# Kernel tuning notes

Hardware: AMD Instinct MI355X
Metric: run time of the kernel (lower is better)

The kernel has to match this reference:

```python
import jax, jax.numpy as jnp
import numpy as np

N, E = 50000, 400000
FN, FE = 128, 128          # in/out node and edge feature dims
W = 256                     # fnns_width
EPS = 1e-5


def _layer_norm(x, g, b):
    m = x.mean(-1, keepdims=True)
    var = x.var(-1, keepdims=True)
    return (x - m) / jnp.sqrt(var + EPS) * g + b


def _fnn(x, params):
    # FNN applies ReLU after EVERY linear, including the last one.
    for w, b in params:
        x = jax.nn.relu(x @ w + b)
    return x


def setup_inputs() -> dict:
    key = jax.random.key(0)
    ks = jax.random.split(key, 32)
    s = 0.05
    d = {
        'v': jax.random.normal(ks[0], (N, FN), jnp.float32),
        'e': jax.random.normal(ks[1], (E, FE), jnp.float32),
        'edge_index': jax.random.randint(ks[2], (2, E), 0, N, jnp.int32),
        # edge branch: LayerNorm over concat width FE + 2*FN = 384
        'edge_ln_g': jnp.ones((FE + 2 * FN,), jnp.float32),
        'edge_ln_b': jnp.zeros((FE + 2 * FN,), jnp.float32),
        'ew0': jax.random.normal(ks[3], (FE + 2 * FN, W), jnp.float32) * s,
        'eb0': jnp.zeros((W,), jnp.float32),
        'ew1': jax.random.normal(ks[4], (W, W), jnp.float32) * s,
        'eb1': jnp.zeros((W,), jnp.float32),
        'ew2': jax.random.normal(ks[5], (W, FE), jnp.float32) * s,
        'eb2': jnp.zeros((FE,), jnp.float32),
        'edge_linear': jax.random.normal(ks[6], (FE, FE), jnp.float32) * s,
        # node branch: LayerNorm over concat width FE + FN = 256
        'node_ln_g': jnp.ones((FE + FN,), jnp.float32),
        'node_ln_b': jnp.zeros((FE + FN,), jnp.float32),
        'nw0': jax.random.normal(ks[7], (FE + FN, W), jnp.float32) * s,
        'nb0': jnp.zeros((W,), jnp.float32),
        'nw1': jax.random.normal(ks[8], (W, W), jnp.float32) * s,
        'nb1': jnp.zeros((W,), jnp.float32),
        'nw2': jax.random.normal(ks[9], (W, FN), jnp.float32) * s,
        'nb2': jnp.zeros((FN,), jnp.float32),
        'node_linear': jax.random.normal(ks[10], (FN, FN), jnp.float32) * s,
    }
    return d


def reference(v, e, edge_index, edge_ln_g, edge_ln_b, ew0, eb0, ew1, eb1,
              ew2, eb2, edge_linear, node_ln_g, node_ln_b, nw0, nb0, nw1,
              nb1, nw2, nb2, node_linear):
    row, col = edge_index[0], edge_index[1]
    n = v.shape[0]
    # edge update: residual linear + FNN(LayerNorm(concat))
    edge_in = jnp.concatenate([e, v[row], v[col]], axis=-1)  # [E, 384]
    e_new = e @ edge_linear + _fnn(
        _layer_norm(edge_in, edge_ln_g, edge_ln_b),
        [(ew0, eb0), (ew1, eb1), (ew2, eb2)])
    # mean scatter-aggregate over destination nodes (col)
    counts = jax.ops.segment_sum(jnp.ones((e.shape[0],), e.dtype), col,
                                 num_segments=n)
    e_aggr = jax.ops.segment_sum(e_new, col, num_segments=n)
    e_aggr = e_aggr / jnp.clip(counts, 1.0)[:, None]
    # node update
    node_in = jnp.concatenate([e_aggr, v], axis=-1)  # [N, 256]
    v_new = v @ node_linear + _fnn(
        _layer_norm(node_in, node_ln_g, node_ln_b),
        [(nw0, nb0), (nw1, nb1), (nw2, nb2)])
    return (v_new, e_new)
```

## Files before the change

kernel.cpp:

```cpp
#include <hip/hip_runtime.h>

typedef _Float16 f16_t;
typedef f16_t f16x4 __attribute__((ext_vector_type(4)));
typedef f16_t f16x8 __attribute__((ext_vector_type(8)));
typedef float f32x4 __attribute__((ext_vector_type(4)));

#define MFMA16(a, b, c) __builtin_amdgcn_mfma_f32_16x16x32_f16((a), (b), (c), 0, 0, 0)

__device__ __forceinline__ float bfr(float x) { return (float)(__bf16)x; }

__global__ void pack_weights_kernel(
    const float* __restrict__ ew0, const float* __restrict__ ew1,
    const float* __restrict__ ew2, const float* __restrict__ eL,
    const float* __restrict__ nw0, const float* __restrict__ nw1,
    const float* __restrict__ nw2, const float* __restrict__ nL,
    f16_t* __restrict__ dst)
{
    int tid = blockIdx.x * 256 + threadIdx.x;
    int fid = tid >> 6, lane = tid & 63;
    const float* src; int Ncols, foff, doff;
    if (fid < 192)      { src = ew0; Ncols = 256; foff = 0;   doff = 0;      }
    else if (fid < 320) { src = ew1; Ncols = 256; foff = 192; doff = 98304;  }
    else if (fid < 384) { src = ew2; Ncols = 128; foff = 320; doff = 163840; }
    else if (fid < 416) { src = eL;  Ncols = 128; foff = 384; doff = 196608; }
    else if (fid < 544) { src = nw0; Ncols = 256; foff = 416; doff = 212992; }
    else if (fid < 672) { src = nw1; Ncols = 256; foff = 544; doff = 278528; }
    else if (fid < 736) { src = nw2; Ncols = 128; foff = 672; doff = 344064; }
    else                { src = nL;  Ncols = 128; foff = 736; doff = 376832; }
    int f = fid - foff;
    int NT = Ncols >> 4;
    int kstep = f / NT, ntile = f - kstep * NT;
    int col = ntile * 16 + (lane & 15);
    int kbase = kstep * 32 + ((lane >> 4) << 3);
    f16x8 out;
    #pragma unroll
    for (int j = 0; j < 8; ++j)
        out[j] = (f16_t)bfr(src[(size_t)(kbase + j) * Ncols + col]);
    *reinterpret_cast<f16x8*>(dst + (size_t)doff + ((size_t)f * 64 + lane) * 8) = out;
}

__launch_bounds__(1024, 8)
__global__ void edge_kernel(
    const float* __restrict__ vfeat, const float* __restrict__ efeat,
    const int* __restrict__ eidx,
    const float* __restrict__ lng, const float* __restrict__ lnb,
    const f16_t* __restrict__ pw,
    const float* __restrict__ b0, const float* __restrict__ b1,
    const float* __restrict__ b2,
    float* __restrict__ out_e, float* __restrict__ aggr, float* __restrict__ cnts,
    int Ee)
{
    __shared__ f16_t X[64 * 392];
    __shared__ f16_t ER[64 * 136];
    __shared__ int cidx[64];

    const int t    = threadIdx.x;
    const int lane = t & 63;
    const int wv   = t >> 6;
    const size_t ebase = (size_t)blockIdx.x * 64;

    const int el = t >> 4;
    const int pp = t & 15;
    const size_t eg = ebase + el;
    const int r0 = eidx[eg];
    const int c0 = eidx[(size_t)Ee + eg];

    float s = 0.f, sq = 0.f;
    {
        const float4* e4 = (const float4*)efeat;
        const float4* v4 = (const float4*)vfeat;
        #pragma unroll
        for (int i = 0; i < 6; ++i) {
            int q = i * 16 + pp;
            float4 r;
            if (q < 32)      r = e4[eg * 32 + q];
            else if (q < 64) r = v4[(size_t)r0 * 32 + (q - 32)];
            else             r = v4[(size_t)c0 * 32 + (q - 64)];
            r.x = bfr(r.x); r.y = bfr(r.y); r.z = bfr(r.z); r.w = bfr(r.w);
            f16x4 h;
            h[0] = (f16_t)r.x; h[1] = (f16_t)r.y; h[2] = (f16_t)r.z; h[3] = (f16_t)r.w;
            *reinterpret_cast<f16x4*>(&X[el * 392 + q * 4]) = h;
            if (q < 32)
                *reinterpret_cast<f16x4*>(&ER[el * 136 + q * 4]) = h;
            s  += r.x + r.y + r.z + r.w;
            sq += r.x*r.x + r.y*r.y + r.z*r.z + r.w*r.w;
        }
        if (pp == 0) {
            cidx[el] = c0;
            unsafeAtomicAdd(&cnts[c0], 1.0f);
        }
    }
    #pragma unroll
    for (int off = 1; off < 16; off <<= 1) {
        s  += __shfl_xor(s, off);
        sq += __shfl_xor(sq, off);
    }
    const float mean = s * (1.f / 384.f);
    const float rstd = 1.f / sqrtf(sq * (1.f / 384.f) - mean * mean + 1e-5f);

    {
        const float4* g4p = (const float4*)lng;
        const float4* bpp = (const float4*)lnb;
        #pragma unroll
        for (int i = 0; i < 6; ++i) {
            int q = i * 16 + pp;
            f16x4 h = *reinterpret_cast<f16x4*>(&X[el * 392 + q * 4]);
            float4 g = g4p[q]; float4 bb = bpp[q];
            h[0] = (f16_t)(((float)h[0] - mean) * rstd * bfr(g.x) + bfr(bb.x));
            h[1] = (f16_t)(((float)h[1] - mean) * rstd * bfr(g.y) + bfr(bb.y));
            h[2] = (f16_t)(((float)h[2] - mean) * rstd * bfr(g.z) + bfr(bb.z));
            h[3] = (f16_t)(((float)h[3] - mean) * rstd * bfr(g.w) + bfr(bb.w));
            *reinterpret_cast<f16x4*>(&X[el * 392 + q * 4]) = h;
        }
    }
    __syncthreads();

    const int r16 = lane & 15;
    const int g4i = lane >> 4;

    {
        f32x4 acc[4] = {};
        const f16_t* bw = pw;
        #pragma unroll
        for (int ks = 0; ks < 12; ++ks) {
            f16x8 b = *reinterpret_cast<const f16x8*>(
                &bw[((size_t)(ks * 16 + wv) * 64 + lane) * 8]);
            #pragma unroll
            for (int m = 0; m < 4; ++m) {
                f16x8 a = *reinterpret_cast<const f16x8*>(
                    &X[(m * 16 + r16) * 392 + ks * 32 + g4i * 8]);
                acc[m] = MFMA16(a, b, acc[m]);
            }
        }
        __syncthreads();
        int c = wv * 16 + r16;
        float bias = bfr(b0[c]);
        #pragma unroll
        for (int m = 0; m < 4; ++m)
            #pragma unroll
            for (int qi = 0; qi < 4; ++qi) {
                int rr = m * 16 + g4i * 4 + qi;
                X[rr * 264 + c] = (f16_t)fmaxf(acc[m][qi] + bias, 0.f);
            }
    }
    __syncthreads();

    {
        f32x4 acc[4] = {};
        const f16_t* bw = pw + 98304;
        #pragma unroll
        for (int ks = 0; ks < 8; ++ks) {
            f16x8 b = *reinterpret_cast<const f16x8*>(
                &bw[((size_t)(ks * 16 + wv) * 64 + lane) * 8]);
            #pragma unroll
            for (int m = 0; m < 4; ++m) {
                f16x8 a = *reinterpret_cast<const f16x8*>(
                    &X[(m * 16 + r16) * 264 + ks * 32 + g4i * 8]);
                acc[m] = MFMA16(a, b, acc[m]);
            }
        }
        __syncthreads();
        int c = wv * 16 + r16;
        float bias = bfr(b1[c]);
        #pragma unroll
        for (int m = 0; m < 4; ++m)
            #pragma unroll
            for (int qi = 0; qi < 4; ++qi) {
                int rr = m * 16 + g4i * 4 + qi;
                X[rr * 264 + c] = (f16_t)fmaxf(acc[m][qi] + bias, 0.f);
            }
    }
    __syncthreads();

    {
        const int nh = wv & 7;
        const int mh = wv >> 3;
        f32x4 accF[2] = {}, accR[2] = {};
        const f16_t* bw = pw + 163840;
        #pragma unroll
        for (int ks = 0; ks < 8; ++ks) {
            f16x8 b = *reinterpret_cast<const f16x8*>(
                &bw[((size_t)(ks * 8 + nh) * 64 + lane) * 8]);
            #pragma unroll
            for (int m = 0; m < 2; ++m) {
                f16x8 a = *reinterpret_cast<const f16x8*>(
                    &X[(mh * 32 + m * 16 + r16) * 264 + ks * 32 + g4i * 8]);
                accF[m] = MFMA16(a, b, accF[m]);
            }
        }
        const f16_t* bwL = pw + 196608;
        #pragma unroll
        for (int ks = 0; ks < 4; ++ks) {
            f16x8 b = *reinterpret_cast<const f16x8*>(
                &bwL[((size_t)(ks * 8 + nh) * 64 + lane) * 8]);
            #pragma unroll
            for (int m = 0; m < 2; ++m) {
                f16x8 a = *reinterpret_cast<const f16x8*>(
                    &ER[(mh * 32 + m * 16 + r16) * 136 + ks * 32 + g4i * 8]);
                accR[m] = MFMA16(a, b, accR[m]);
            }
        }
        int c = nh * 16 + r16;
        float bias = bfr(b2[c]);
        #pragma unroll
        for (int m = 0; m < 2; ++m)
            #pragma unroll
            for (int qi = 0; qi < 4; ++qi) {
                int rr = mh * 32 + m * 16 + g4i * 4 + qi;
                float val = accR[m][qi] + fmaxf(accF[m][qi] + bias, 0.f);
                size_t eg2 = ebase + rr;
                out_e[eg2 * 128 + c] = val;
                unsafeAtomicAdd(&aggr[(size_t)cidx[rr] * 128 + c], val);
            }
    }
}

__launch_bounds__(512, 6)
__global__ void node_kernel(
    const float* __restrict__ vfeat, const float* __restrict__ aggr,
    const float* __restrict__ cnts,
    const float* __restrict__ lng, const float* __restrict__ lnb,
    const f16_t* __restrict__ pw,
    const float* __restrict__ b0, const float* __restrict__ b1,
    const float* __restrict__ b2,
    float* __restrict__ out_v, int Nn)
{
    __shared__ f16_t X[32 * 264];
    __shared__ f16_t H1[32 * 264];

    const int t    = threadIdx.x;
    const int lane = t & 63;
    const int wv   = t >> 6;
    const size_t nbase = (size_t)blockIdx.x * 32;

    const int nl = t >> 4;
    const int pp = t & 15;
    const size_t ng = nbase + nl;
    const bool valid = ng < (size_t)Nn;

    float4 d[4];
    float s = 0.f, sq = 0.f;
    {
        float cmax = 1.f;
        if (valid) cmax = fmaxf(cnts[ng], 1.f);
        const float4* a4 = (const float4*)aggr;
        const float4* v4 = (const float4*)vfeat;
        #pragma unroll
        for (int i = 0; i < 4; ++i) {
            int q = i * 16 + pp;
            float4 r = make_float4(0.f, 0.f, 0.f, 0.f);
            if (valid) {
                if (q < 32) {
                    r = a4[ng * 32 + q];
                    r.x = r.x / cmax; r.y = r.y / cmax;
                    r.z = r.z / cmax; r.w = r.w / cmax;
                } else {
                    float4 rv = v4[ng * 32 + (q - 32)];
                    r.x = bfr(rv.x); r.y = bfr(rv.y); r.z = bfr(rv.z); r.w = bfr(rv.w);
                }
            }
            d[i] = r;
            s  += r.x + r.y + r.z + r.w;
            sq += r.x*r.x + r.y*r.y + r.z*r.z + r.w*r.w;
        }
    }
    #pragma unroll
    for (int off = 1; off < 16; off <<= 1) {
        s  += __shfl_xor(s, off);
        sq += __shfl_xor(sq, off);
    }
    const float mean = s * (1.f / 256.f);
    const float rstd = 1.f / sqrtf(sq * (1.f / 256.f) - mean * mean + 1e-5f);
    {
        const float4* g4p = (const float4*)lng;
        const float4* bpp = (const float4*)lnb;
        #pragma unroll
        for (int i = 0; i < 4; ++i) {
            int q = i * 16 + pp;
            float4 g = g4p[q]; float4 bb = bpp[q];
            f16x4 y;
            y[0] = (f16_t)((d[i].x - mean) * rstd * bfr(g.x) + bfr(bb.x));
            y[1] = (f16_t)((d[i].y - mean) * rstd * bfr(g.y) + bfr(bb.y));
            y[2] = (f16_t)((d[i].z - mean) * rstd * bfr(g.z) + bfr(bb.z));
            y[3] = (f16_t)((d[i].w - mean) * rstd * bfr(g.w) + bfr(bb.w));
            *reinterpret_cast<f16x4*>(&X[nl * 264 + q * 4]) = y;
        }
    }
    __syncthreads();

    const int r16 = lane & 15;
    const int g4i = lane >> 4;

    {
        f32x4 acc[2][2] = {};
        const f16_t* bw = pw;
        #pragma unroll
        for (int ks = 0; ks < 8; ++ks) {
            f16x8 a0 = *reinterpret_cast<const f16x8*>(&X[r16 * 264 + ks * 32 + g4i * 8]);
            f16x8 a1 = *reinterpret_cast<const f16x8*>(&X[(16 + r16) * 264 + ks * 32 + g4i * 8]);
            #pragma unroll
            for (int n = 0; n < 2; ++n) {
                f16x8 b = *reinterpret_cast<const f16x8*>(
                    &bw[((size_t)(ks * 16 + wv * 2 + n) * 64 + lane) * 8]);
                acc[0][n] = MFMA16(a0, b, acc[0][n]);
                acc[1][n] = MFMA16(a1, b, acc[1][n]);
            }
        }
        #pragma unroll
        for (int n = 0; n < 2; ++n) {
            int c = wv * 32 + n * 16 + r16;
            float bias = bfr(b0[c]);
            #pragma unroll
            for (int m = 0; m < 2; ++m)
                #pragma unroll
                for (int qi = 0; qi < 4; ++qi) {
                    int rr = m * 16 + g4i * 4 + qi;
                    H1[rr * 264 + c] = (f16_t)fmaxf(acc[m][n][qi] + bias, 0.f);
                }
        }
    }
    __syncthreads();

    f16_t* h2 = X;
    {
        f32x4 acc[2][2] = {};
        const f16_t* bw = pw + 65536;
        #pragma unroll
        for (int ks = 0; ks < 8; ++ks) {
            f16x8 a0 = *reinterpret_cast<const f16x8*>(&H1[r16 * 264 + ks * 32 + g4i * 8]);
            f16x8 a1 = *reinterpret_cast<const f16x8*>(&H1[(16 + r16) * 264 + ks * 32 + g4i * 8]);
            #pragma unroll
            for (int n = 0; n < 2; ++n) {
                f16x8 b = *reinterpret_cast<const f16x8*>(
                    &bw[((size_t)(ks * 16 + wv * 2 + n) * 64 + lane) * 8]);
                acc[0][n] = MFMA16(a0, b, acc[0][n]);
                acc[1][n] = MFMA16(a1, b, acc[1][n]);
            }
        }
        __syncthreads();
        #pragma unroll
        for (int n = 0; n < 2; ++n) {
            int c = wv * 32 + n * 16 + r16;
            float bias = bfr(b1[c]);
            #pragma unroll
            for (int m = 0; m < 2; ++m)
                #pragma unroll
                for (int qi = 0; qi < 4; ++qi) {
                    int rr = m * 16 + g4i * 4 + qi;
                    h2[rr * 264 + c] = (f16_t)fmaxf(acc[m][n][qi] + bias, 0.f);
                }
        }
    }
    __syncthreads();

    {
        f32x4 accF[2] = {}, accR[2] = {};
        const f16_t* bw = pw + 131072;
        #pragma unroll
        for (int ks = 0; ks < 8; ++ks) {
            f16x8 a0 = *reinterpret_cast<const f16x8*>(&h2[r16 * 264 + ks * 32 + g4i * 8]);
            f16x8 a1 = *reinterpret_cast<const f16x8*>(&h2[(16 + r16) * 264 + ks * 32 + g4i * 8]);
            f16x8 b = *reinterpret_cast<const f16x8*>(
                &bw[((size_t)(ks * 8 + wv) * 64 + lane) * 8]);
            accF[0] = MFMA16(a0, b, accF[0]);
            accF[1] = MFMA16(a1, b, accF[1]);
        }
        const f16_t* bwL = pw + 163840;
        #pragma unroll
        for (int ks = 0; ks < 4; ++ks) {
            f16x8 a[2];
            #pragma unroll
            for (int m = 0; m < 2; ++m) {
                size_t rv = nbase + (size_t)(m * 16 + r16);
                if (rv >= (size_t)Nn) rv = (size_t)Nn - 1;
                const float* src = &vfeat[rv * 128 + ks * 32 + g4i * 8];
                float4 f0 = *(const float4*)src;
                float4 f1 = *(const float4*)(src + 4);
                f16x8 av;
                av[0] = (f16_t)bfr(f0.x); av[1] = (f16_t)bfr(f0.y);
                av[2] = (f16_t)bfr(f0.z); av[3] = (f16_t)bfr(f0.w);
                av[4] = (f16_t)bfr(f1.x); av[5] = (f16_t)bfr(f1.y);
                av[6] = (f16_t)bfr(f1.z); av[7] = (f16_t)bfr(f1.w);
                a[m] = av;
            }
            f16x8 b = *reinterpret_cast<const f16x8*>(
                &bwL[((size_t)(ks * 8 + wv) * 64 + lane) * 8]);
            accR[0] = MFMA16(a[0], b, accR[0]);
            accR[1] = MFMA16(a[1], b, accR[1]);
        }
        int c = wv * 16 + r16;
        float bias = bfr(b2[c]);
        #pragma unroll
        for (int m = 0; m < 2; ++m)
            #pragma unroll
            for (int qi = 0; qi < 4; ++qi) {
                int rr = m * 16 + g4i * 4 + qi;
                size_t ng2 = nbase + rr;
                if (ng2 < (size_t)Nn) {
                    float val = accR[m][qi] + fmaxf(accF[m][qi] + bias, 0.f);
                    out_v[ng2 * 128 + c] = val;
                }
            }
    }
}

extern "C" void kernel_launch(void* const* d_in, const int* in_sizes, int n_in,
                              void* d_out, int out_size, void* d_ws, size_t ws_size,
                              hipStream_t stream)
{
    const float* v    = (const float*)d_in[0];
    const float* e    = (const float*)d_in[1];
    const int*   eidx = (const int*)d_in[2];
    const float* elng = (const float*)d_in[3];
    const float* elnb = (const float*)d_in[4];
    const float* ew0  = (const float*)d_in[5];
    const float* eb0  = (const float*)d_in[6];
    const float* ew1  = (const float*)d_in[7];
    const float* eb1  = (const float*)d_in[8];
    const float* ew2  = (const float*)d_in[9];
    const float* eb2  = (const float*)d_in[10];
    const float* eLin = (const float*)d_in[11];
    const float* nlng = (const float*)d_in[12];
    const float* nlnb = (const float*)d_in[13];
    const float* nw0  = (const float*)d_in[14];
    const float* nb0  = (const float*)d_in[15];
    const float* nw1  = (const float*)d_in[16];
    const float* nb1  = (const float*)d_in[17];
    const float* nw2  = (const float*)d_in[18];
    const float* nb2  = (const float*)d_in[19];
    const float* nLin = (const float*)d_in[20];

    const int Nn = in_sizes[0] / 128;
    const int Ee = in_sizes[1] / 128;

    float* out_v = (float*)d_out;
    float* out_e = out_v + (size_t)Nn * 128;

    float* aggr = (float*)d_ws;
    float* cnts = aggr + (size_t)Nn * 128;
    f16_t* packw = (f16_t*)((char*)d_ws + (size_t)Nn * 129 * 4);

    hipMemsetAsync(d_ws, 0, (size_t)Nn * 129 * 4, stream);

    pack_weights_kernel<<<192, 256, 0, stream>>>(ew0, ew1, ew2, eLin,
                                                 nw0, nw1, nw2, nLin, packw);

    edge_kernel<<<(Ee + 63) / 64, 1024, 0, stream>>>(v, e, eidx, elng, elnb, packw,
                                                     eb0, eb1, eb2, out_e, aggr, cnts, Ee);

    node_kernel<<<(Nn + 31) / 32, 512, 0, stream>>>(v, aggr, cnts, nlng, nlnb,
                                                    packw + 212992, nb0, nb1, nb2,
                                                    out_v, Nn);
}
```

Baseline: 436.0 us.

## Swap MFMA operands to emit transposed tiles with vectorized stores and drop ER buffer

The MFMA operands are swapped so weights go in the A slot and activations in the B slot. Each lane then holds four consecutive output columns for one row, which allows f16x4 stores into shared memory and float4 stores to global output in place of scalar stores. The edge kernel also drops the ER shared-memory copy of the raw edge features and re-reads them from global memory for the residual linear, which shrinks LDS use and may raise occupancy. The cost is extra global loads for the residual path, and the aggregation atomics now hit four adjacent addresses per lane.

```diff
diff --git a/kernel.cpp b/kernel.cpp
--- a/kernel.cpp
+++ b/kernel.cpp
@@ -51,7 +51,6 @@
     int Ee)
 {
     __shared__ f16_t X[64 * 392];
-    __shared__ f16_t ER[64 * 136];
     __shared__ int cidx[64];
 
     const int t    = threadIdx.x;
@@ -61,9 +60,9 @@
 
     const int el = t >> 4;
     const int pp = t & 15;
-    const size_t eg = ebase + el;
-    const int r0 = eidx[eg];
-    const int c0 = eidx[(size_t)Ee + eg];
+    const size_t eg0 = ebase + el;
+    const int r0 = eidx[eg0];
+    const int c0 = eidx[(size_t)Ee + eg0];
 
     float s = 0.f, sq = 0.f;
     {
@@ -73,15 +72,13 @@
         for (int i = 0; i < 6; ++i) {
             int q = i * 16 + pp;
             float4 r;
-            if (q < 32)      r = e4[eg * 32 + q];
+            if (q < 32)      r = e4[eg0 * 32 + q];
             else if (q < 64) r = v4[(size_t)r0 * 32 + (q - 32)];
             else             r = v4[(size_t)c0 * 32 + (q - 64)];
             r.x = bfr(r.x); r.y = bfr(r.y); r.z = bfr(r.z); r.w = bfr(r.w);
             f16x4 h;
             h[0] = (f16_t)r.x; h[1] = (f16_t)r.y; h[2] = (f16_t)r.z; h[3] = (f16_t)r.w;
             *reinterpret_cast<f16x4*>(&X[el * 392 + q * 4]) = h;
-            if (q < 32)
-                *reinterpret_cast<f16x4*>(&ER[el * 136 + q * 4]) = h;
             s  += r.x + r.y + r.z + r.w;
             sq += r.x*r.x + r.y*r.y + r.z*r.z + r.w*r.w;
         }
@@ -117,31 +114,34 @@
 
     const int r16 = lane & 15;
     const int g4i = lane >> 4;
+    const int cb4 = g4i * 4;
 
     {
         f32x4 acc[4] = {};
         const f16_t* bw = pw;
         #pragma unroll
         for (int ks = 0; ks < 12; ++ks) {
-            f16x8 b = *reinterpret_cast<const f16x8*>(
+            f16x8 wa = *reinterpret_cast<const f16x8*>(
                 &bw[((size_t)(ks * 16 + wv) * 64 + lane) * 8]);
             #pragma unroll
-            for (int m = 0; m < 4; ++m) {
-                f16x8 a = *reinterpret_cast<const f16x8*>(
-                    &X[(m * 16 + r16) * 392 + ks * 32 + g4i * 8]);
-                acc[m] = MFMA16(a, b, acc[m]);
+            for (int et = 0; et < 4; ++et) {
+                f16x8 xb = *reinterpret_cast<const f16x8*>(
+                    &X[(et * 16 + r16) * 392 + ks * 32 + g4i * 8]);
+                acc[et] = MFMA16(wa, xb, acc[et]);
             }
         }
         __syncthreads();
-        int c = wv * 16 + r16;
-        float bias = bfr(b0[c]);
-        #pragma unroll
-        for (int m = 0; m < 4; ++m)
-            #pragma unroll
-            for (int qi = 0; qi < 4; ++qi) {
-                int rr = m * 16 + g4i * 4 + qi;
-                X[rr * 264 + c] = (f16_t)fmaxf(acc[m][qi] + bias, 0.f);
-            }
+        int cb = wv * 16 + cb4;
+        float4 bs = *reinterpret_cast<const float4*>(&b0[cb]);
+        float bias[4] = { bfr(bs.x), bfr(bs.y), bfr(bs.z), bfr(bs.w) };
+        #pragma unroll
+        for (int et = 0; et < 4; ++et) {
+            f16x4 hv;
+            #pragma unroll
+            for (int qi = 0; qi < 4; ++qi)
+                hv[qi] = (f16_t)fmaxf(acc[et][qi] + bias[qi], 0.f);
+            *reinterpret_cast<f16x4*>(&X[(et * 16 + r16) * 264 + cb]) = hv;
+        }
     }
     __syncthreads();
 
@@ -150,25 +150,27 @@
         const f16_t* bw = pw + 98304;
         #pragma unroll
         for (int ks = 0; ks < 8; ++ks) {
-            f16x8 b = *reinterpret_cast<const f16x8*>(
+            f16x8 wa = *reinterpret_cast<const f16x8*>(
                 &bw[((size_t)(ks * 16 + wv) * 64 + lane) * 8]);
             #pragma unroll
-            for (int m = 0; m < 4; ++m) {
-                f16x8 a = *reinterpret_cast<const f16x8*>(
-                    &X[(m * 16 + r16) * 264 + ks * 32 + g4i * 8]);
-                acc[m] = MFMA16(a, b, acc[m]);
+            for (int et = 0; et < 4; ++et) {
+                f16x8 xb = *reinterpret_cast<const f16x8*>(
+                    &X[(et * 16 + r16) * 264 + ks * 32 + g4i * 8]);
+                acc[et] = MFMA16(wa, xb, acc[et]);
             }
         }
         __syncthreads();
-        int c = wv * 16 + r16;
-        float bias = bfr(b1[c]);
-        #pragma unroll
-        for (int m = 0; m < 4; ++m)
-            #pragma unroll
-            for (int qi = 0; qi < 4; ++qi) {
-                int rr = m * 16 + g4i * 4 + qi;
-                X[rr * 264 + c] = (f16_t)fmaxf(acc[m][qi] + bias, 0.f);
-            }
+        int cb = wv * 16 + cb4;
+        float4 bs = *reinterpret_cast<const float4*>(&b1[cb]);
+        float bias[4] = { bfr(bs.x), bfr(bs.y), bfr(bs.z), bfr(bs.w) };
+        #pragma unroll
+        for (int et = 0; et < 4; ++et) {
+            f16x4 hv;
+            #pragma unroll
+            for (int qi = 0; qi < 4; ++qi)
+                hv[qi] = (f16_t)fmaxf(acc[et][qi] + bias[qi], 0.f);
+            *reinterpret_cast<f16x4*>(&X[(et * 16 + r16) * 264 + cb]) = hv;
+        }
     }
     __syncthreads();
 
@@ -179,39 +181,53 @@
         const f16_t* bw = pw + 163840;
         #pragma unroll
         for (int ks = 0; ks < 8; ++ks) {
-            f16x8 b = *reinterpret_cast<const f16x8*>(
+            f16x8 wa = *reinterpret_cast<const f16x8*>(
                 &bw[((size_t)(ks * 8 + nh) * 64 + lane) * 8]);
             #pragma unroll
-            for (int m = 0; m < 2; ++m) {
-                f16x8 a = *reinterpret_cast<const f16x8*>(
-                    &X[(mh * 32 + m * 16 + r16) * 264 + ks * 32 + g4i * 8]);
-                accF[m] = MFMA16(a, b, accF[m]);
+            for (int p = 0; p < 2; ++p) {
+                f16x8 xb = *reinterpret_cast<const f16x8*>(
+                    &X[((mh * 2 + p) * 16 + r16) * 264 + ks * 32 + g4i * 8]);
+                accF[p] = MFMA16(wa, xb, accF[p]);
             }
         }
         const f16_t* bwL = pw + 196608;
         #pragma unroll
         for (int ks = 0; ks < 4; ++ks) {
-            f16x8 b = *reinterpret_cast<const f16x8*>(
+            f16x8 wa = *reinterpret_cast<const f16x8*>(
                 &bwL[((size_t)(ks * 8 + nh) * 64 + lane) * 8]);
             #pragma unroll
-            for (int m = 0; m < 2; ++m) {
-                f16x8 a = *reinterpret_cast<const f16x8*>(
-                    &ER[(mh * 32 + m * 16 + r16) * 136 + ks * 32 + g4i * 8]);
-                accR[m] = MFMA16(a, b, accR[m]);
-            }
-        }
-        int c = nh * 16 + r16;
-        float bias = bfr(b2[c]);
-        #pragma unroll
-        for (int m = 0; m < 2; ++m)
-            #pragma unroll
-            for (int qi = 0; qi < 4; ++qi) {
-                int rr = mh * 32 + m * 16 + g4i * 4 + qi;
-                float val = accR[m][qi] + fmaxf(accF[m][qi] + bias, 0.f);
-                size_t eg2 = ebase + rr;
-                out_e[eg2 * 128 + c] = val;
-                unsafeAtomicAdd(&aggr[(size_t)cidx[rr] * 128 + c], val);
-            }
+            for (int p = 0; p < 2; ++p) {
+                size_t er = ebase + (size_t)((mh * 2 + p) * 16 + r16);
+                const float4* src = (const float4*)&efeat[er * 128 + ks * 32 + g4i * 8];
+                float4 f0 = src[0];
+                float4 f1 = src[1];
+                f16x8 ebf;
+                ebf[0] = (f16_t)bfr(f0.x); ebf[1] = (f16_t)bfr(f0.y);
+                ebf[2] = (f16_t)bfr(f0.z); ebf[3] = (f16_t)bfr(f0.w);
+                ebf[4] = (f16_t)bfr(f1.x); ebf[5] = (f16_t)bfr(f1.y);
+                ebf[6] = (f16_t)bfr(f1.z); ebf[7] = (f16_t)bfr(f1.w);
+                accR[p] = MFMA16(wa, ebf, accR[p]);
+            }
+        }
+        int cb = nh * 16 + cb4;
+        float4 bs = *reinterpret_cast<const float4*>(&b2[cb]);
+        float bias[4] = { bfr(bs.x), bfr(bs.y), bfr(bs.z), bfr(bs.w) };
+        #pragma unroll
+        for (int p = 0; p < 2; ++p) {
+            int rr = (mh * 2 + p) * 16 + r16;
+            size_t eg2 = ebase + rr;
+            float4 val;
+            val.x = accR[p][0] + fmaxf(accF[p][0] + bias[0], 0.f);
+            val.y = accR[p][1] + fmaxf(accF[p][1] + bias[1], 0.f);
+            val.z = accR[p][2] + fmaxf(accF[p][2] + bias[2], 0.f);
+            val.w = accR[p][3] + fmaxf(accF[p][3] + bias[3], 0.f);
+            *reinterpret_cast<float4*>(&out_e[eg2 * 128 + cb]) = val;
+            float* ap = &aggr[(size_t)cidx[rr] * 128 + cb];
+            unsafeAtomicAdd(ap + 0, val.x);
+            unsafeAtomicAdd(ap + 1, val.y);
+            unsafeAtomicAdd(ap + 2, val.z);
+            unsafeAtomicAdd(ap + 3, val.w);
+        }
     }
 }
 
@@ -290,65 +306,73 @@
 
     const int r16 = lane & 15;
     const int g4i = lane >> 4;
+    const int cb4 = g4i * 4;
 
     {
         f32x4 acc[2][2] = {};
         const f16_t* bw = pw;
         #pragma unroll
         for (int ks = 0; ks < 8; ++ks) {
-            f16x8 a0 = *reinterpret_cast<const f16x8*>(&X[r16 * 264 + ks * 32 + g4i * 8]);
-            f16x8 a1 = *reinterpret_cast<const f16x8*>(&X[(16 + r16) * 264 + ks * 32 + g4i * 8]);
-            #pragma unroll
-            for (int n = 0; n < 2; ++n) {
-                f16x8 b = *reinterpret_cast<const f16x8*>(
-                    &bw[((size_t)(ks * 16 + wv * 2 + n) * 64 + lane) * 8]);
-                acc[0][n] = MFMA16(a0, b, acc[0][n]);
-                acc[1][n] = MFMA16(a1, b, acc[1][n]);
-            }
-        }
-        #pragma unroll
-        for (int n = 0; n < 2; ++n) {
-            int c = wv * 32 + n * 16 + r16;
-            float bias = bfr(b0[c]);
-            #pragma unroll
-            for (int m = 0; m < 2; ++m)
+            f16x8 wa0 = *reinterpret_cast<const f16x8*>(
+                &bw[((size_t)(ks * 16 + wv * 2 + 0) * 64 + lane) * 8]);
+            f16x8 wa1 = *reinterpret_cast<const f16x8*>(
+                &bw[((size_t)(ks * 16 + wv * 2 + 1) * 64 + lane) * 8]);
+            #pragma unroll
+            for (int nt = 0; nt < 2; ++nt) {
+                f16x8 xb = *reinterpret_cast<const f16x8*>(
+                    &X[(nt * 16 + r16) * 264 + ks * 32 + g4i * 8]);
+                acc[nt][0] = MFMA16(wa0, xb, acc[nt][0]);
+                acc[nt][1] = MFMA16(wa1, xb, acc[nt][1]);
+            }
+        }
+        #pragma unroll
+        for (int j = 0; j < 2; ++j) {
+            int cb = (wv * 2 + j) * 16 + cb4;
+            float4 bs = *reinterpret_cast<const float4*>(&b0[cb]);
+            float bias[4] = { bfr(bs.x), bfr(bs.y), bfr(bs.z), bfr(bs.w) };
+            #pragma unroll
+            for (int nt = 0; nt < 2; ++nt) {
+                f16x4 hv;
                 #pragma unroll
-                for (int qi = 0; qi < 4; ++qi) {
-                    int rr = m * 16 + g4i * 4 + qi;
-                    H1[rr * 264 + c] = (f16_t)fmaxf(acc[m][n][qi] + bias, 0.f);
-                }
-        }
-    }
-    __syncthreads();
-
-    f16_t* h2 = X;
+                for (int qi = 0; qi < 4; ++qi)
+                    hv[qi] = (f16_t)fmaxf(acc[nt][j][qi] + bias[qi], 0.f);
+                *reinterpret_cast<f16x4*>(&H1[(nt * 16 + r16) * 264 + cb]) = hv;
+            }
+        }
+    }
+    __syncthreads();
+
     {
         f32x4 acc[2][2] = {};
         const f16_t* bw = pw + 65536;
         #pragma unroll
         for (int ks = 0; ks < 8; ++ks) {
-            f16x8 a0 = *reinterpret_cast<const f16x8*>(&H1[r16 * 264 + ks * 32 + g4i * 8]);
-            f16x8 a1 = *reinterpret_cast<const f16x8*>(&H1[(16 + r16) * 264 + ks * 32 + g4i * 8]);
-            #pragma unroll
-            for (int n = 0; n < 2; ++n) {
-                f16x8 b = *reinterpret_cast<const f16x8*>(
-                    &bw[((size_t)(ks * 16 + wv * 2 + n) * 64 + lane) * 8]);
-                acc[0][n] = MFMA16(a0, b, acc[0][n]);
-                acc[1][n] = MFMA16(a1, b, acc[1][n]);
+            f16x8 wa0 = *reinterpret_cast<const f16x8*>(
+                &bw[((size_t)(ks * 16 + wv * 2 + 0) * 64 + lane) * 8]);
+            f16x8 wa1 = *reinterpret_cast<const f16x8*>(
+                &bw[((size_t)(ks * 16 + wv * 2 + 1) * 64 + lane) * 8]);
+            #pragma unroll
+            for (int nt = 0; nt < 2; ++nt) {
+                f16x8 xb = *reinterpret_cast<const f16x8*>(
+                    &H1[(nt * 16 + r16) * 264 + ks * 32 + g4i * 8]);
+                acc[nt][0] = MFMA16(wa0, xb, acc[nt][0]);
+                acc[nt][1] = MFMA16(wa1, xb, acc[nt][1]);
             }
         }
         __syncthreads();
         #pragma unroll
-        for (int n = 0; n < 2; ++n) {
-            int c = wv * 32 + n * 16 + r16;
-            float bias = bfr(b1[c]);
-            #pragma unroll
-            for (int m = 0; m < 2; ++m)
+        for (int j = 0; j < 2; ++j) {
+            int cb = (wv * 2 + j) * 16 + cb4;
+            float4 bs = *reinterpret_cast<const float4*>(&b1[cb]);
+            float bias[4] = { bfr(bs.x), bfr(bs.y), bfr(bs.z), bfr(bs.w) };
+            #pragma unroll
+            for (int nt = 0; nt < 2; ++nt) {
+                f16x4 hv;
                 #pragma unroll
-                for (int qi = 0; qi < 4; ++qi) {
-                    int rr = m * 16 + g4i * 4 + qi;
-                    h2[rr * 264 + c] = (f16_t)fmaxf(acc[m][n][qi] + bias, 0.f);
-                }
+                for (int qi = 0; qi < 4; ++qi)
+                    hv[qi] = (f16_t)fmaxf(acc[nt][j][qi] + bias[qi], 0.f);
+                *reinterpret_cast<f16x4*>(&X[(nt * 16 + r16) * 264 + cb]) = hv;
+            }
         }
     }
     __syncthreads();
@@ -358,49 +382,50 @@
         const f16_t* bw = pw + 131072;
         #pragma unroll
         for (int ks = 0; ks < 8; ++ks) {
-            f16x8 a0 = *reinterpret_cast<const f16x8*>(&h2[r16 * 264 + ks * 32 + g4i * 8]);
-            f16x8 a1 = *reinterpret_cast<const f16x8*>(&h2[(16 + r16) * 264 + ks * 32 + g4i * 8]);
-            f16x8 b = *reinterpret_cast<const f16x8*>(
+            f16x8 wa = *reinterpret_cast<const f16x8*>(
                 &bw[((size_t)(ks * 8 + wv) * 64 + lane) * 8]);
-            accF[0] = MFMA16(a0, b, accF[0]);
-            accF[1] = MFMA16(a1, b, accF[1]);
+            #pragma unroll
+            for (int nt = 0; nt < 2; ++nt) {
+                f16x8 xb = *reinterpret_cast<const f16x8*>(
+                    &X[(nt * 16 + r16) * 264 + ks * 32 + g4i * 8]);
+                accF[nt] = MFMA16(wa, xb, accF[nt]);
+            }
         }
         const f16_t* bwL = pw + 163840;
         #pragma unroll
         for (int ks = 0; ks < 4; ++ks) {
-            f16x8 a[2];
-            #pragma unroll
-            for (int m = 0; m < 2; ++m) {
-                size_t rv = nbase + (size_t)(m * 16 + r16);
+            f16x8 wa = *reinterpret_cast<const f16x8*>(
+                &bwL[((size_t)(ks * 8 + wv) * 64 + lane) * 8]);
+            #pragma unroll
+            for (int nt = 0; nt < 2; ++nt) {
+                size_t rv = nbase + (size_t)(nt * 16 + r16);
                 if (rv >= (size_t)Nn) rv = (size_t)Nn - 1;
-                const float* src = &vfeat[rv * 128 + ks * 32 + g4i * 8];
-                float4 f0 = *(const float4*)src;
-                float4 f1 = *(const float4*)(src + 4);
-                f16x8 av;
-                av[0] = (f16_t)bfr(f0.x); av[1] = (f16_t)bfr(f0.y);
-                av[2] = (f16_t)bfr(f0.z); av[3] = (f16_t)bfr(f0.w);
-                av[4] = (f16_t)bfr(f1.x); av[5] = (f16_t)bfr(f1.y);
-                av[6] = (f16_t)bfr(f1.z); av[7] = (f16_t)bfr(f1.w);
-                a[m] = av;
-            }
-            f16x8 b = *reinterpret_cast<const f16x8*>(
-                &bwL[((size_t)(ks * 8 + wv) * 64 + lane) * 8]);
-            accR[0] = MFMA16(a[0], b, accR[0]);
-            accR[1] = MFMA16(a[1], b, accR[1]);
-        }
-        int c = wv * 16 + r16;
-        float bias = bfr(b2[c]);
-        #pragma unroll
-        for (int m = 0; m < 2; ++m)
-            #pragma unroll
-            for (int qi = 0; qi < 4; ++qi) {
-                int rr = m * 16 + g4i * 4 + qi;
-                size_t ng2 = nbase + rr;
-                if (ng2 < (size_t)Nn) {
-                    float val = accR[m][qi] + fmaxf(accF[m][qi] + bias, 0.f);
-                    out_v[ng2 * 128 + c] = val;
-                }
-            }
+                const float4* src = (const float4*)&vfeat[rv * 128 + ks * 32 + g4i * 8];
+                float4 f0 = src[0];
+                float4 f1 = src[1];
+                f16x8 vb;
+                vb[0] = (f16_t)bfr(f0.x); vb[1] = (f16_t)bfr(f0.y);
+                vb[2] = (f16_t)bfr(f0.z); vb[3] = (f16_t)bfr(f0.w);
+                vb[4] = (f16_t)bfr(f1.x); vb[5] = (f16_t)bfr(f1.y);
+                vb[6] = (f16_t)bfr(f1.z); vb[7] = (f16_t)bfr(f1.w);
+                accR[nt] = MFMA16(wa, vb, accR[nt]);
+            }
+        }
+        int cb = wv * 16 + cb4;
+        float4 bs = *reinterpret_cast<const float4*>(&b2[cb]);
+        float bias[4] = { bfr(bs.x), bfr(bs.y), bfr(bs.z), bfr(bs.w) };
+        #pragma unroll
+        for (int nt = 0; nt < 2; ++nt) {
+            size_t ng2 = nbase + (size_t)(nt * 16 + r16);
+            if (ng2 < (size_t)Nn) {
+                float4 val;
+                val.x = accR[nt][0] + fmaxf(accF[nt][0] + bias[0], 0.f);
+                val.y = accR[nt][1] + fmaxf(accF[nt][1] + bias[1], 0.f);
+                val.z = accR[nt][2] + fmaxf(accF[nt][2] + bias[2], 0.f);
+                val.w = accR[nt][3] + fmaxf(accF[nt][3] + bias[3], 0.f);
+                *reinterpret_cast<float4*>(&out_v[ng2 * 128 + cb]) = val;
+            }
+        }
     }
 }
 
```

Measured after the change: 930.0 us. +113.3%, slower.
